# Kernel optimization log

Hardware: AMD Instinct MI355X
Metric: run time of the kernel (lower is better)

Reference implementation:

```python
import jax, jax.numpy as jnp
import numpy as np
from jax.ops import segment_sum, segment_max

N = 400000          # points
V = 100000          # occupied voxels
EPS = 1e-3          # BN eps from norm_cfg
VX, VY, VZ = 0.2, 0.2, 4.0          # voxel_size
X0, Y0, Z0 = 0.0, -40.0, -3.0       # point_cloud_range mins
GX, GY, GZ = 352, 400, 1            # grid dims


def setup_inputs() -> dict:
    key = jax.random.key(0)
    ks = jax.random.split(key, 12)
    # points: xyz uniform inside the point cloud range, 4th channel = intensity
    xyz = jax.random.uniform(ks[0], (N, 3), jnp.float32) \
        * jnp.array([70.4, 80.0, 4.0], jnp.float32) \
        + jnp.array([X0, Y0, Z0], jnp.float32)
    inten = jax.random.uniform(ks[1], (N, 1), jnp.float32)
    features = jnp.concatenate([xyz, inten], axis=1)
    # point -> voxel mapping; guarantee every voxel id occupied so
    # segment_max semantics match torch's unique-voxel reduce exactly
    inv = jnp.concatenate([jnp.arange(V, dtype=jnp.int32),
                           jax.random.randint(ks[2], (N - V,), 0, V, jnp.int32)])
    inv = jax.random.permutation(ks[3], inv)
    # voxel coordinates (batch, z, y, x)
    b = jax.random.randint(ks[4], (V,), 0, 2, jnp.int32)
    z = jnp.zeros((V,), jnp.int32)
    y = jax.random.randint(ks[5], (V,), 0, GY, jnp.int32)
    x = jax.random.randint(ks[6], (V,), 0, GX, jnp.int32)
    coors = jnp.stack([b, z, y, x], axis=1)
    # VFE params: Linear(bias=False) + BN1d(gamma, beta)
    W0 = jax.random.normal(ks[7], (64, 10), jnp.float32) * (1.0 / np.sqrt(10))
    W1 = jax.random.normal(ks[8], (64, 128), jnp.float32) * (1.0 / np.sqrt(128))
    return dict(features=features, W0=W0,
                gamma0=jnp.ones((64,), jnp.float32), beta0=jnp.zeros((64,), jnp.float32),
                W1=W1,
                gamma1=jnp.ones((64,), jnp.float32), beta1=jnp.zeros((64,), jnp.float32),
                inv=inv, coors=coors)


def _bn_relu(x, gamma, beta):
    # BN1d in training mode: biased batch stats over the point dim
    mu = jnp.mean(x, axis=0)
    var = jnp.var(x, axis=0)
    return jax.nn.relu(gamma * (x - mu) * jax.lax.rsqrt(var + EPS) + beta)


def _stats(xyz, inv, coors):
    # cluster-center offset: per-voxel mean of xyz, gathered back
    cnt = segment_sum(jnp.ones((xyz.shape[0],), xyz.dtype), inv, num_segments=V)
    mean = segment_sum(xyz, inv, num_segments=V) / cnt[:, None]
    f_cluster = xyz - mean[inv]
    # voxel-center offset: coors order is (batch, z, y, x)
    cf = coors.astype(xyz.dtype)
    center = jnp.stack([cf[:, 3] * VX + VX / 2 + X0,
                        cf[:, 2] * VY + VY / 2 + Y0,
                        cf[:, 1] * VZ + VZ / 2 + Z0], axis=1)
    f_center = xyz - center[inv]
    return jnp.concatenate([xyz, f_cluster, f_center], axis=1)  # [N, 9]


def reference(features, W0, gamma0, beta0, W1, gamma1, beta1, inv, coors):
    x = jnp.concatenate([_stats(features[:, :3], inv, coors), features[:, 3:]], axis=1)  # [N,10]
    # VFE layer 0
    h0 = _bn_relu(x @ W0.T, gamma0, beta0)                     # [N,64]
    v0 = segment_max(h0, inv, num_segments=V)                  # [V,64]
    x1 = jnp.concatenate([h0, v0[inv]], axis=1)                # [N,128]
    # VFE layer 1
    h1 = _bn_relu(x1 @ W1.T, gamma1, beta1)                    # [N,64]
    voxel_feats = segment_max(h1, inv, num_segments=V)         # [V,64]
    return voxel_feats, coors
```

## Files before the change

### kernel.cpp

```cpp
#include <hip/hip_runtime.h>
#include <hip/hip_bf16.h>

#define NPTS 400000
#define NVOX 100000
#define EPSB 1e-3f
#define NTILE 6250
#define NBLK_SCAN 391
#define GBLK 782

#define OFF_ACC4   0
#define OFF_GRAM   (4*NVOX)
#define OFF_STATS  (OFF_GRAM + 72)
#define OFF_P1     (OFF_STATS + 256)
#define OFF_V0     (OFF_P1 + 4096)
#define OFF_Y1M    (OFF_V0 + NVOX*64)
#define ZERO_FLOATS (OFF_Y1M + NVOX*64)
#define OFF_VTMP   ZERO_FLOATS
#define OFF_BSUM   (OFF_VTMP + NVOX)
#define OFF_VOFF   (OFF_BSUM + 512)
#define OFF_VSTART (OFF_VOFF + NVOX)
#define OFF_ORD    (OFF_VSTART + NVOX + 8)
#define OFF_VS     (OFF_ORD + NPTS)
#define OFF_W0F    (OFF_VS + NPTS)
#define OFF_W1B    (OFF_W0F + 640)
#define OFF_H0T    (OFF_W1B + 4096)

#define S_SC0 0
#define S_BI0 64

#define XTB_LD 136
#define HT_LD  65

typedef __bf16 bf16x8 __attribute__((ext_vector_type(8)));
typedef float  f32x4  __attribute__((ext_vector_type(4)));

__device__ __forceinline__ float b2f(__hip_bfloat16 h) { return __bfloat162float(h); }
__device__ __forceinline__ float bfbits2f(unsigned short u) {
    return __uint_as_float((unsigned int)u << 16);
}
__device__ __forceinline__ unsigned short bf16u(float f) {
    __hip_bfloat16 h = __float2bfloat16(f);
    return __builtin_bit_cast(unsigned short, h);
}
__device__ __forceinline__ unsigned int fkey(float f) {
    unsigned int u = __float_as_uint(f);
    return (u & 0x80000000u) ? ~u : (u | 0x80000000u);
}
__device__ __forceinline__ float funkey(unsigned int k) {
    unsigned int u = (k & 0x80000000u) ? (k & 0x7FFFFFFFu) : ~k;
    return __uint_as_float(u);
}

__device__ __forceinline__ void compute_x(const __hip_bfloat16* __restrict__ feat,
                                          const float* __restrict__ acc4,
                                          const int* __restrict__ coors,
                                          long i, int v, float* xv) {
    ushort4 f4 = *(const ushort4*)(feat + 4 * i);
    float px = bfbits2f(f4.x), py = bfbits2f(f4.y), pz = bfbits2f(f4.z), it = bfbits2f(f4.w);
    float4 a4 = *(const float4*)&acc4[4 * (long)v];
    float ic = 1.0f / a4.x;
    int4 c4 = *(const int4*)&coors[4 * (long)v];
    xv[0] = px; xv[1] = py; xv[2] = pz;
    xv[3] = px - a4.y * ic; xv[4] = py - a4.z * ic; xv[5] = pz - a4.w * ic;
    xv[6] = px - ((float)c4.w * 0.2f + 0.1f);
    xv[7] = py - ((float)c4.z * 0.2f + 0.1f - 40.0f);
    xv[8] = pz - ((float)c4.y * 4.0f + 2.0f - 3.0f);
    xv[9] = it;
}

__global__ void k_vsum(const __hip_bfloat16* __restrict__ feat,
                       const int* __restrict__ inv,
                       float* __restrict__ acc4,
                       const __hip_bfloat16* __restrict__ W0,
                       const __hip_bfloat16* __restrict__ W1,
                       float* __restrict__ W0f, unsigned short* __restrict__ w1b) {
    if (blockIdx.x == 6250) {
        int t = threadIdx.x;
        for (int j = t; j < 640; j += 256) W0f[j] = b2f(W0[j]);
        for (int f = t; f < 8192; f += 256) {
            int j  = f & 7;
            int l  = (f >> 3) & 63;
            int ks = (f >> 9) & 3;
            int ct = f >> 11;
            int ch = ct * 16 + (l & 15);
            int k  = ks * 32 + ((l >> 4) & 3) * 8 + j;
            w1b[f] = __builtin_bit_cast(unsigned short, W1[ch * 128 + k]);
        }
        return;
    }
    long t = (long)blockIdx.x * 256 + threadIdx.x;
    int pt = (int)(t >> 2);
    int comp = (int)(t & 3);
    float val = (comp == 0) ? 1.0f : b2f(feat[4 * pt + comp - 1]);
    int v = inv[pt];
    atomicAdd(&acc4[(long)v * 4 + comp], val);
}

__global__ void k_scan1(const float* __restrict__ acc4,
                        int* __restrict__ vtmp, int* __restrict__ bsum) {
    __shared__ int sc[256];
    int b = blockIdx.x, t = threadIdx.x;
    int v = b * 256 + t;
    int c = (v < NVOX) ? (int)acc4[4 * (long)v] : 0;
    sc[t] = c;
    __syncthreads();
    int val = c;
    for (int off = 1; off < 256; off <<= 1) {
        int x = (t >= off) ? sc[t - off] : 0;
        __syncthreads();
        val += x; sc[t] = val;
        __syncthreads();
    }
    if (v < NVOX) vtmp[v] = val - c;
    if (t == 255) bsum[b] = val;
}

__global__ void k_scan2(int* __restrict__ bsum) {
    __shared__ int sc[512];
    int t = threadIdx.x;
    int c = (t < NBLK_SCAN) ? bsum[t] : 0;
    sc[t] = c;
    __syncthreads();
    int val = c;
    for (int off = 1; off < 512; off <<= 1) {
        int x = (t >= off) ? sc[t - off] : 0;
        __syncthreads();
        val += x; sc[t] = val;
        __syncthreads();
    }
    if (t < NBLK_SCAN) bsum[t] = val - c;
}

__global__ void k_scan3(const int* __restrict__ vtmp, const int* __restrict__ bsum,
                        int* __restrict__ voff, int* __restrict__ vstart) {
    int v = blockIdx.x * 256 + threadIdx.x;
    if (v < NVOX) {
        int s = vtmp[v] + bsum[v >> 8];
        voff[v] = s;
        vstart[v] = s;
    }
    if (v == 0) vstart[NVOX] = NPTS;
}

__global__ __launch_bounds__(256, 4)
void k_prep(const __hip_bfloat16* __restrict__ feat,
            const int* __restrict__ inv,
            const int* __restrict__ coors,
            const float* __restrict__ acc4,
            int* __restrict__ voff,
            int* __restrict__ ord, int* __restrict__ vsorted,
            float* __restrict__ gram) {
    __shared__ float gs[72];
    int t = threadIdx.x;
    if (t < 72) gs[t] = 0.0f;
    __syncthreads();

    float sx[10], sxx[55];
#pragma unroll
    for (int a = 0; a < 10; a++) sx[a] = 0.0f;
#pragma unroll
    for (int a = 0; a < 55; a++) sxx[a] = 0.0f;

    for (long i = (long)blockIdx.x * 256 + t; i < NPTS; i += (long)GBLK * 256) {
        int v = inv[i];
        float xv[10];
        compute_x(feat, acc4, coors, i, v, xv);
        int idx = 0;
#pragma unroll
        for (int a = 0; a < 10; a++) {
            sx[a] += xv[a];
#pragma unroll
            for (int b = 0; b <= a; b++) sxx[idx++] += xv[a] * xv[b];
        }
        int pos = atomicAdd(&voff[v], 1);
        ord[pos] = (int)i;
        vsorted[pos] = v;
    }

#pragma unroll
    for (int v = 0; v < 65; v++) {
        float s = (v < 10) ? sx[v] : sxx[v - 10];
        for (int m = 32; m >= 1; m >>= 1) s += __shfl_xor(s, m);
        if ((t & 63) == 0) atomicAdd(&gs[v], s);
    }
    __syncthreads();
    if (t < 65) atomicAdd(&gram[t], gs[t]);
}

__global__ void k_finalize0(const float* __restrict__ gram,
                            const float* __restrict__ W0f,
                            const __hip_bfloat16* __restrict__ gamma,
                            const __hip_bfloat16* __restrict__ beta,
                            float* __restrict__ stats) {
    int c = threadIdx.x;
    if (c >= 64) return;
    float w[10];
#pragma unroll
    for (int k = 0; k < 10; k++) w[k] = W0f[c*10 + k];
    float sum = 0.0f, sq = 0.0f;
#pragma unroll
    for (int a = 0; a < 10; a++) {
        sum += w[a] * gram[a];
        float ta = 0.0f;
#pragma unroll
        for (int b = 0; b < 10; b++) {
            int hi = (a >= b) ? a : b, lo = (a >= b) ? b : a;
            ta += w[b] * gram[10 + hi*(hi+1)/2 + lo];
        }
        sq += w[a] * ta;
    }
    float mu  = sum * (1.0f / NPTS);
    float var = sq * (1.0f / NPTS) - mu * mu;
    float g   = b2f(gamma[c]) * rsqrtf(var + EPSB);
    stats[S_SC0 + c] = g;
    stats[S_BI0 + c] = b2f(beta[c]) - mu * g;
}

__global__ __launch_bounds__(256, 6)
void k_h0max(const int* __restrict__ ord, const int* __restrict__ vsorted,
             const int* __restrict__ vstart,
             const __hip_bfloat16* __restrict__ feat,
             const float* __restrict__ acc4, const int* __restrict__ coors,
             const float* __restrict__ W0f, const float* __restrict__ stats,
             float* __restrict__ v0, unsigned short* __restrict__ h0t) {
    __shared__ float ht[64 * HT_LD];
    __shared__ int invs[64];
    int t = threadIdx.x, w = t >> 6, l = t & 63;
    int base = blockIdx.x * 64;
    int i = ord[base + l];
    int v = vsorted[base + l];
    if (w == 0) invs[l] = v;

    float xv[10];
    compute_x(feat, acc4, coors, (long)i, v, xv);
    int cw = w * 16;
#pragma unroll
    for (int j = 0; j < 16; j++) {
        int c = cw + j;
        float y = 0.0f;
#pragma unroll
        for (int k = 0; k < 10; k++) y += xv[k] * W0f[c*10 + k];
        ht[l * HT_LD + c] = fmaxf(stats[S_SC0 + c] * y + stats[S_BI0 + c], 0.0f);
    }
    __syncthreads();

#pragma unroll
    for (int u = 0; u < 2; u++) {
        int idx = t + u * 256;
        int pt2 = idx >> 3;
        int c0 = (idx & 7) * 8;
        const float* src = &ht[pt2 * HT_LD + c0];
        float4 a  = *(const float4*)src;
        float4 b4 = *(const float4*)(src + 4);
        uint4 o;
        o.x = (unsigned int)bf16u(a.x)  | ((unsigned int)bf16u(a.y)  << 16);
        o.y = (unsigned int)bf16u(a.z)  | ((unsigned int)bf16u(a.w)  << 16);
        o.z = (unsigned int)bf16u(b4.x) | ((unsigned int)bf16u(b4.y) << 16);
        o.w = (unsigned int)bf16u(b4.z) | ((unsigned int)bf16u(b4.w) << 16);
        *(uint4*)&h0t[(long)(base + pt2) * 64 + c0] = o;
    }

    unsigned int mk = 0u;
#pragma unroll
    for (int j = 0; j < 16; j++) {
        int p = cw + j;
        unsigned int hb = __float_as_uint(ht[p * HT_LD + l]);
        mk = (hb > mk) ? hb : mk;
        if (j == 15 || invs[p + 1] != invs[p]) {
            int vv = invs[p];
            int s0 = vstart[vv], s1 = vstart[vv + 1];
            unsigned int* dst = (unsigned int*)&v0[(long)vv * 64 + l];
            if (s0 >= base + cw && s1 <= base + cw + 16)
                *dst = mk;
            else
                atomicMax(dst, mk);
            mk = 0u;
        }
    }
}

__global__ __launch_bounds__(256, 6)
void k_mfma_stats(const int* __restrict__ vsorted,
                  const int* __restrict__ vstart,
                  const unsigned short* __restrict__ h0t,
                  const unsigned short* __restrict__ w1b,
                  const float* __restrict__ v0,
                  float* __restrict__ P1,
                  unsigned int* __restrict__ y1m) {
    __shared__ union {
        unsigned short xtb[64 * XTB_LD];
        float ht[64 * HT_LD];
    } sm;
    __shared__ int invs[64];
    int t = threadIdx.x, w = t >> 6, l = t & 63;
    int quad = l >> 4, lm = l & 15;
    int base = blockIdx.x * 64;
    if (w == 0) invs[l] = vsorted[base + l];

    bf16x8 bfrag[4];
    const uint4* wf = (const uint4*)w1b;
#pragma unroll
    for (int ks = 0; ks < 4; ks++)
        bfrag[ks] = __builtin_bit_cast(bf16x8, wf[(w * 4 + ks) * 64 + l]);

#pragma unroll
    for (int u = 0; u < 2; u++) {
        int idx = t + u * 256;
        int pt = idx >> 3, c0 = (idx & 7) * 8;
        uint4 d = *(const uint4*)&h0t[(long)(base + pt) * 64 + c0];
        *(uint4*)&sm.xtb[pt * XTB_LD + c0] = d;
    }
    {
        int p = t >> 2, q = t & 3;
        int vv = vsorted[base + p];
        const float4* src = (const float4*)&v0[(long)vv * 64 + q * 16];
#pragma unroll
        for (int u = 0; u < 4; u++) {
            float4 f4 = src[u];
            ushort4 s4 = { bf16u(f4.x), bf16u(f4.y), bf16u(f4.z), bf16u(f4.w) };
            *(ushort4*)&sm.xtb[p * XTB_LD + 64 + q * 16 + 4 * u] = s4;
        }
    }
    __syncthreads();

    f32x4 acc[4];
#pragma unroll
    for (int pg = 0; pg < 4; pg++) acc[pg] = (f32x4){0.f, 0.f, 0.f, 0.f};
#pragma unroll
    for (int ks = 0; ks < 4; ks++) {
#pragma unroll
        for (int pg = 0; pg < 4; pg++) {
            const uint4* ap = (const uint4*)&sm.xtb[(pg * 16 + lm) * XTB_LD + ks * 32 + quad * 8];
            bf16x8 a = __builtin_bit_cast(bf16x8, *ap);
            acc[pg] = __builtin_amdgcn_mfma_f32_16x16x32_bf16(a, bfrag[ks], acc[pg], 0, 0, 0);
        }
    }

    float ssum = 0.0f, ssq = 0.0f;
#pragma unroll
    for (int pg = 0; pg < 4; pg++) {
#pragma unroll
        for (int r = 0; r < 4; r++) {
            float y = acc[pg][r];
            ssum += y; ssq += y * y;
        }
    }
    __syncthreads();

#pragma unroll
    for (int pg = 0; pg < 4; pg++) {
#pragma unroll
        for (int r = 0; r < 4; r++)
            sm.ht[(pg * 16 + quad * 4 + r) * HT_LD + w * 16 + lm] = acc[pg][r];
    }
    __syncthreads();

    unsigned int mk = 0u;
    int cw = w * 16;
#pragma unroll
    for (int j = 0; j < 16; j++) {
        int p = cw + j;
        unsigned int k2 = fkey(sm.ht[p * HT_LD + l]);
        mk = (k2 > mk) ? k2 : mk;
        if (j == 15 || invs[p + 1] != invs[p]) {
            int vv = invs[p];
            int s0 = vstart[vv], s1 = vstart[vv + 1];
            unsigned int* dst = &y1m[(long)vv * 64 + l];
            if (s0 >= base + cw && s1 <= base + cw + 16)
                *dst = mk;
            else
                atomicMax(dst, mk);
            mk = 0u;
        }
    }

    ssum += __shfl_xor(ssum, 16); ssq += __shfl_xor(ssq, 16);
    ssum += __shfl_xor(ssum, 32); ssq += __shfl_xor(ssq, 32);
    if (l < 16) {
        int slot = blockIdx.x & 31;
        atomicAdd(&P1[slot * 128 + w * 16 + lm], ssum);
        atomicAdd(&P1[slot * 128 + 64 + w * 16 + lm], ssq);
    }
}

#define OUTBLK 512
__global__ __launch_bounds__(256)
void k_out(const unsigned int* __restrict__ y1m,
           const float* __restrict__ P1,
           const __hip_bfloat16* __restrict__ gamma,
           const __hip_bfloat16* __restrict__ beta,
           const int* __restrict__ coors,
           float* __restrict__ out) {
    __shared__ float sc1s[64], bi1s[64];
    int t = threadIdx.x;
    if (t < 64) {
        float sum = 0.0f, sq = 0.0f;
        for (int s = 0; s < 32; s++) {
            sum += P1[s*128 + t];
            sq  += P1[s*128 + 64 + t];
        }
        float mu  = sum * (1.0f / NPTS);
        float var = sq * (1.0f / NPTS) - mu * mu;
        float g   = b2f(gamma[t]) * rsqrtf(var + EPSB);
        sc1s[t] = g;
        bi1s[t] = b2f(beta[t]) - mu * g;
    }
    __syncthreads();

    const long n4feat = (long)NVOX * 16;
    const long n4all  = n4feat + NVOX;
    const long nfeat  = (long)NVOX * 64;
    for (long idx = (long)blockIdx.x * 256 + t; idx < n4all; idx += (long)OUTBLK * 256) {
        if (idx < n4feat) {
            uint4 kk = ((const uint4*)y1m)[idx];
            int c0 = (int)((idx * 4) & 63);
            float4 o;
            o.x = fmaxf(sc1s[c0+0] * funkey(kk.x) + bi1s[c0+0], 0.0f);
            o.y = fmaxf(sc1s[c0+1] * funkey(kk.y) + bi1s[c0+1], 0.0f);
            o.z = fmaxf(sc1s[c0+2] * funkey(kk.z) + bi1s[c0+2], 0.0f);
            o.w = fmaxf(sc1s[c0+3] * funkey(kk.w) + bi1s[c0+3], 0.0f);
            ((float4*)out)[idx] = o;
        } else {
            long vi = idx - n4feat;
            int4 c4 = ((const int4*)coors)[vi];
            float4 o;
            o.x = b2f(__float2bfloat16((float)c4.x));
            o.y = b2f(__float2bfloat16((float)c4.y));
            o.z = b2f(__float2bfloat16((float)c4.z));
            o.w = b2f(__float2bfloat16((float)c4.w));
            ((float4*)(out + nfeat))[vi] = o;
        }
    }
}

extern "C" void kernel_launch(void* const* d_in, const int* in_sizes, int n_in,
                              void* d_out, int out_size, void* d_ws, size_t ws_size,
                              hipStream_t stream) {
    const __hip_bfloat16* feat = (const __hip_bfloat16*)d_in[0];
    const __hip_bfloat16* W0   = (const __hip_bfloat16*)d_in[1];
    const __hip_bfloat16* g0   = (const __hip_bfloat16*)d_in[2];
    const __hip_bfloat16* be0  = (const __hip_bfloat16*)d_in[3];
    const __hip_bfloat16* W1   = (const __hip_bfloat16*)d_in[4];
    const __hip_bfloat16* g1   = (const __hip_bfloat16*)d_in[5];
    const __hip_bfloat16* be1  = (const __hip_bfloat16*)d_in[6];
    const int* inv   = (const int*)d_in[7];
    const int* coors = (const int*)d_in[8];
    float* out = (float*)d_out;

    float* ws    = (float*)d_ws;
    float* acc4  = ws + OFF_ACC4;
    float* gram  = ws + OFF_GRAM;
    float* stats = ws + OFF_STATS;
    float* P1    = ws + OFF_P1;
    float* v0    = ws + OFF_V0;
    unsigned int* y1m = (unsigned int*)(ws + OFF_Y1M);
    int* vtmp    = (int*)(ws + OFF_VTMP);
    int* bsum    = (int*)(ws + OFF_BSUM);
    int* voff    = (int*)(ws + OFF_VOFF);
    int* vstart  = (int*)(ws + OFF_VSTART);
    int* ord     = (int*)(ws + OFF_ORD);
    int* vsorted = (int*)(ws + OFF_VS);
    float* W0f   = ws + OFF_W0F;
    unsigned short* w1b = (unsigned short*)(ws + OFF_W1B);
    unsigned short* h0t = (unsigned short*)(ws + OFF_H0T);

    hipMemsetAsync(ws, 0, (size_t)ZERO_FLOATS * sizeof(float), stream);

    k_vsum<<<6251, 256, 0, stream>>>(feat, inv, acc4, W0, W1, W0f, w1b);
    k_scan1<<<NBLK_SCAN, 256, 0, stream>>>(acc4, vtmp, bsum);
    k_scan2<<<1, 512, 0, stream>>>(bsum);
    k_scan3<<<NBLK_SCAN, 256, 0, stream>>>(vtmp, bsum, voff, vstart);
    k_prep<<<GBLK, 256, 0, stream>>>(feat, inv, coors, acc4, voff, ord, vsorted, gram);
    k_finalize0<<<1, 64, 0, stream>>>(gram, W0f, g0, be0, stats);
    k_h0max<<<NTILE, 256, 0, stream>>>(ord, vsorted, vstart, feat, acc4, coors,
                                       W0f, stats, v0, h0t);
    k_mfma_stats<<<NTILE, 256, 0, stream>>>(vsorted, vstart, h0t, w1b, v0, P1, y1m);
    k_out<<<OUTBLK, 256, 0, stream>>>(y1m, P1, g1, be1, coors, out);
}
```

Measured before the change: 264.0 us.

## Shrink workspace memset, zero only atomically-reduced voxels, fuse BN0 finalize into h0max

The big memset no longer clears the v0 and y1m buffers (2×V×64 floats). Instead, k_scan3 zeros rows only for voxels whose sorted point range crosses a 16-point group boundary, since those are the only rows written with atomicMax rather than a direct store. The separate single-block k_finalize0 launch is removed. Each k_h0max block now recomputes the BN0 scale and bias from the Gram matrix in one wave while another wave computes the per-point x features. Launch bounds for the two main kernels rise from 6 to 8 waves/blocks per SM, which risks register spills, and the per-block stat recompute adds redundant work.

Measured after the change: 265.9 us. Within noise of the previous version (+0.7%).

```diff
diff --git a/kernel.cpp b/kernel.cpp
--- a/kernel.cpp
+++ b/kernel.cpp
@@ -12,10 +12,10 @@
 #define OFF_GRAM   (4*NVOX)
 #define OFF_STATS  (OFF_GRAM + 72)
 #define OFF_P1     (OFF_STATS + 256)
-#define OFF_V0     (OFF_P1 + 4096)
+#define ZERO_FLOATS (OFF_P1 + 4096)
+#define OFF_V0     ZERO_FLOATS
 #define OFF_Y1M    (OFF_V0 + NVOX*64)
-#define ZERO_FLOATS (OFF_Y1M + NVOX*64)
-#define OFF_VTMP   ZERO_FLOATS
+#define OFF_VTMP   (OFF_Y1M + NVOX*64)
 #define OFF_BSUM   (OFF_VTMP + NVOX)
 #define OFF_VOFF   (OFF_BSUM + 512)
 #define OFF_VSTART (OFF_VOFF + NVOX)
@@ -24,9 +24,6 @@
 #define OFF_W0F    (OFF_VS + NPTS)
 #define OFF_W1B    (OFF_W0F + 640)
 #define OFF_H0T    (OFF_W1B + 4096)
-
-#define S_SC0 0
-#define S_BI0 64
 
 #define XTB_LD 136
 #define HT_LD  65
@@ -132,12 +129,23 @@
 }
 
 __global__ void k_scan3(const int* __restrict__ vtmp, const int* __restrict__ bsum,
-                        int* __restrict__ voff, int* __restrict__ vstart) {
+                        int* __restrict__ voff, int* __restrict__ vstart,
+                        float* __restrict__ v0, unsigned int* __restrict__ y1m) {
     int v = blockIdx.x * 256 + threadIdx.x;
     if (v < NVOX) {
-        int s = vtmp[v] + bsum[v >> 8];
-        voff[v] = s;
-        vstart[v] = s;
+        int s0 = vtmp[v] + bsum[v >> 8];
+        voff[v] = s0;
+        vstart[v] = s0;
+        int s1;
+        if (v + 1 < NVOX) s1 = vtmp[v + 1] + bsum[(v + 1) >> 8];
+        else              s1 = NPTS;
+        if ((s0 >> 4) != ((s1 - 1) >> 4)) {
+            float4 z4 = {0.f, 0.f, 0.f, 0.f};
+            float4* pv = (float4*)&v0[(long)v * 64];
+            float4* py = (float4*)&y1m[(long)v * 64];
+#pragma unroll
+            for (int u = 0; u < 16; u++) { pv[u] = z4; py[u] = z4; }
+        }
     }
     if (v == 0) vstart[NVOX] = NPTS;
 }
@@ -187,60 +195,66 @@
     if (t < 65) atomicAdd(&gram[t], gs[t]);
 }
 
-__global__ void k_finalize0(const float* __restrict__ gram,
-                            const float* __restrict__ W0f,
-                            const __hip_bfloat16* __restrict__ gamma,
-                            const __hip_bfloat16* __restrict__ beta,
-                            float* __restrict__ stats) {
-    int c = threadIdx.x;
-    if (c >= 64) return;
-    float w[10];
-#pragma unroll
-    for (int k = 0; k < 10; k++) w[k] = W0f[c*10 + k];
-    float sum = 0.0f, sq = 0.0f;
-#pragma unroll
-    for (int a = 0; a < 10; a++) {
-        sum += w[a] * gram[a];
-        float ta = 0.0f;
-#pragma unroll
-        for (int b = 0; b < 10; b++) {
-            int hi = (a >= b) ? a : b, lo = (a >= b) ? b : a;
-            ta += w[b] * gram[10 + hi*(hi+1)/2 + lo];
-        }
-        sq += w[a] * ta;
-    }
-    float mu  = sum * (1.0f / NPTS);
-    float var = sq * (1.0f / NPTS) - mu * mu;
-    float g   = b2f(gamma[c]) * rsqrtf(var + EPSB);
-    stats[S_SC0 + c] = g;
-    stats[S_BI0 + c] = b2f(beta[c]) - mu * g;
-}
-
-__global__ __launch_bounds__(256, 6)
+__global__ __launch_bounds__(256, 8)
 void k_h0max(const int* __restrict__ ord, const int* __restrict__ vsorted,
              const int* __restrict__ vstart,
              const __hip_bfloat16* __restrict__ feat,
              const float* __restrict__ acc4, const int* __restrict__ coors,
-             const float* __restrict__ W0f, const float* __restrict__ stats,
+             const float* __restrict__ W0f, const float* __restrict__ gram,
+             const __hip_bfloat16* __restrict__ g0,
+             const __hip_bfloat16* __restrict__ be0,
              float* __restrict__ v0, unsigned short* __restrict__ h0t) {
     __shared__ float ht[64 * HT_LD];
     __shared__ int invs[64];
+    __shared__ float xvs[640];
+    __shared__ float sc0s[64], bi0s[64];
     int t = threadIdx.x, w = t >> 6, l = t & 63;
     int base = blockIdx.x * 64;
-    int i = ord[base + l];
-    int v = vsorted[base + l];
-    if (w == 0) invs[l] = v;
+
+    if (w == 0) {
+        int i = ord[base + l];
+        int v = vsorted[base + l];
+        invs[l] = v;
+        float xv[10];
+        compute_x(feat, acc4, coors, (long)i, v, xv);
+#pragma unroll
+        for (int k = 0; k < 10; k++) xvs[k * 64 + l] = xv[k];
+    } else if (w == 1) {
+        int c = l;
+        float wr[10];
+#pragma unroll
+        for (int k = 0; k < 10; k++) wr[k] = W0f[c * 10 + k];
+        float sum = 0.0f, sq = 0.0f;
+#pragma unroll
+        for (int a = 0; a < 10; a++) {
+            sum += wr[a] * gram[a];
+            float ta = 0.0f;
+#pragma unroll
+            for (int b = 0; b < 10; b++) {
+                int hi = (a >= b) ? a : b, lo = (a >= b) ? b : a;
+                ta += wr[b] * gram[10 + hi * (hi + 1) / 2 + lo];
+            }
+            sq += wr[a] * ta;
+        }
+        float mu  = sum * (1.0f / NPTS);
+        float var = sq * (1.0f / NPTS) - mu * mu;
+        float g   = b2f(g0[c]) * rsqrtf(var + EPSB);
+        sc0s[c] = g;
+        bi0s[c] = b2f(be0[c]) - mu * g;
+    }
+    __syncthreads();
 
     float xv[10];
-    compute_x(feat, acc4, coors, (long)i, v, xv);
+#pragma unroll
+    for (int k = 0; k < 10; k++) xv[k] = xvs[k * 64 + l];
     int cw = w * 16;
 #pragma unroll
     for (int j = 0; j < 16; j++) {
         int c = cw + j;
         float y = 0.0f;
 #pragma unroll
-        for (int k = 0; k < 10; k++) y += xv[k] * W0f[c*10 + k];
-        ht[l * HT_LD + c] = fmaxf(stats[S_SC0 + c] * y + stats[S_BI0 + c], 0.0f);
+        for (int k = 0; k < 10; k++) y += xv[k] * W0f[c * 10 + k];
+        ht[l * HT_LD + c] = fmaxf(sc0s[c] * y + bi0s[c], 0.0f);
     }
     __syncthreads();
 
@@ -279,7 +293,7 @@
     }
 }
 
-__global__ __launch_bounds__(256, 6)
+__global__ __launch_bounds__(256, 8)
 void k_mfma_stats(const int* __restrict__ vsorted,
                   const int* __restrict__ vstart,
                   const unsigned short* __restrict__ h0t,
@@ -450,7 +464,6 @@
     float* ws    = (float*)d_ws;
     float* acc4  = ws + OFF_ACC4;
     float* gram  = ws + OFF_GRAM;
-    float* stats = ws + OFF_STATS;
     float* P1    = ws + OFF_P1;
     float* v0    = ws + OFF_V0;
     unsigned int* y1m = (unsigned int*)(ws + OFF_Y1M);
@@ -469,11 +482,10 @@
     k_vsum<<<6251, 256, 0, stream>>>(feat, inv, acc4, W0, W1, W0f, w1b);
     k_scan1<<<NBLK_SCAN, 256, 0, stream>>>(acc4, vtmp, bsum);
     k_scan2<<<1, 512, 0, stream>>>(bsum);
-    k_scan3<<<NBLK_SCAN, 256, 0, stream>>>(vtmp, bsum, voff, vstart);
+    k_scan3<<<NBLK_SCAN, 256, 0, stream>>>(vtmp, bsum, voff, vstart, v0, y1m);
     k_prep<<<GBLK, 256, 0, stream>>>(feat, inv, coors, acc4, voff, ord, vsorted, gram);
-    k_finalize0<<<1, 64, 0, stream>>>(gram, W0f, g0, be0, stats);
     k_h0max<<<NTILE, 256, 0, stream>>>(ord, vsorted, vstart, feat, acc4, coors,
-                                       W0f, stats, v0, h0t);
+                                       W0f, gram, g0, be0, v0, h0t);
     k_mfma_stats<<<NTILE, 256, 0, stream>>>(vsorted, vstart, h0t, w1b, v0, P1, y1m);
     k_out<<<OUTBLK, 256, 0, stream>>>(y1m, P1, g1, be1, coors, out);
 }
```
